# Performance work log

Measured on AMD Instinct MI355X. Metric: run time of the kernel, lower is better.

## Reference

```python
import jax, jax.numpy as jnp
import numpy as np

N = 100000; E = 200000; H = 64; P2 = 250000; P3 = 500000; G = 2048; NC = 10
NF = 18; EF = 18; Y = 0.25; EPS_BN = 1e-5


def setup_inputs() -> dict:
    key = jax.random.key(0)
    ks = jax.random.split(key, 20)
    def rn(i, shape, s=0.05):
        return jax.random.normal(ks[i], shape, jnp.float32) * s
    inp = {}
    inp["x"] = jax.random.normal(ks[0], (N, NF), jnp.float32)
    inp["edge_attr"] = jax.random.normal(ks[1], (E, EF), jnp.float32)
    inp["paths2"] = jax.random.randint(ks[2], (P2, 2), 0, N, jnp.int32)
    inp["ei2"] = jax.random.randint(ks[3], (P2, 1), 0, E, jnp.int32)
    inp["paths3"] = jax.random.randint(ks[4], (P3, 3), 0, N, jnp.int32)
    inp["ei3"] = jax.random.randint(ks[5], (P3, 2), 0, E, jnp.int32)
    inp["batch"] = jnp.sort(jax.random.randint(ks[6], (N,), 0, G, jnp.int32))
    inp["w_feat"] = rn(7, (NF, H)); inp["b_feat"] = jnp.zeros((H,), jnp.float32)
    inp["w_bond"] = rn(8, (EF, H)); inp["b_bond"] = jnp.zeros((H,), jnp.float32)
    inp["w_ih"] = rn(9, (4 * H, 2 * H)); inp["w_hh"] = rn(10, (4 * H, H))
    inp["b_ih"] = jnp.zeros((4 * H,), jnp.float32); inp["b_hh"] = jnp.zeros((4 * H,), jnp.float32)
    inp["bn_g"] = jnp.ones((2, H), jnp.float32); inp["bn_b"] = jnp.zeros((2, H), jnp.float32)
    inp["mlp_w1"] = rn(11, (2, H, H)); inp["mlp_b1"] = jnp.zeros((2, H), jnp.float32)
    inp["bn1_g"] = jnp.ones((2, H), jnp.float32); inp["bn1_b"] = jnp.zeros((2, H), jnp.float32)
    inp["mlp_w2"] = rn(12, (2, H, H)); inp["mlp_b2"] = jnp.zeros((2, H), jnp.float32)
    inp["bn2_g"] = jnp.ones((2, H), jnp.float32); inp["bn2_b"] = jnp.zeros((2, H), jnp.float32)
    inp["w_att"] = rn(13, (H,)); inp["b_att"] = jnp.zeros((1,), jnp.float32)
    inp["w_l1"] = rn(14, (H, H)); inp["b_l1"] = jnp.zeros((H,), jnp.float32)
    inp["w_l2"] = rn(15, (H, NC)); inp["b_l2"] = jnp.zeros((NC,), jnp.float32)
    return inp


def _batch_norm(x, g, b):
    # training-mode BN: biased batch statistics, eps=1e-5 (torch BatchNorm1d)
    m = x.mean(axis=0)
    v = x.var(axis=0)
    return (x - m) * jax.lax.rsqrt(v + EPS_BN) * g + b


def _lstm_final(x_seq, w_ih, w_hh, b_ih, b_hh):
    # x_seq: [P, L, 2H]; torch LSTM gate order i,f,g,o; return final hidden [P, H]
    P = x_seq.shape[0]
    Hd = w_hh.shape[1]
    def step(carry, xt):
        h, c = carry
        gates = xt @ w_ih.T + b_ih + h @ w_hh.T + b_hh
        i, f, g, o = jnp.split(gates, 4, axis=-1)
        c = jax.nn.sigmoid(f) * c + jax.nn.sigmoid(i) * jnp.tanh(g)
        h = jax.nn.sigmoid(o) * jnp.tanh(c)
        return (h, c), None
    h0 = jnp.zeros((P, Hd), x_seq.dtype)
    (h, _), _ = jax.lax.scan(step, (h0, h0), jnp.swapaxes(x_seq, 0, 1))
    return h


def _conv(i, x_in, ea_enc, paths, ei, w_ih, w_hh, b_ih, b_hh, bn_g, bn_b,
          mlp_w1, mlp_b1, bn1_g, bn1_b, mlp_w2, mlp_b2, bn2_g, bn2_b):
    P = paths.shape[0]
    ea = ea_enc[ei]                                        # [P, L-1, H]
    ea = jnp.concatenate([jnp.zeros((P, 1, H), ea.dtype), ea], axis=1)  # [P, L, H]
    x_cat = jnp.concatenate([x_in[paths], ea], axis=-1)    # [P, L, 2H]
    h = _lstm_final(x_cat, w_ih, w_hh, b_ih, b_hh)         # [P, H]
    h = jax.ops.segment_sum(h, paths[:, -1], num_segments=N)  # scatter_add to nodes
    h = _batch_norm(h, bn_g[i], bn_b[i])                   # residuals=False
    h = jax.nn.relu(_batch_norm(h @ mlp_w1[i] + mlp_b1[i], bn1_g[i], bn1_b[i]))
    h = jax.nn.relu(_batch_norm(h @ mlp_w2[i] + mlp_b2[i], bn2_g[i], bn2_b[i]))
    return h


def _attention(query, keys, w_att, b_att):
    scores = []
    for k in keys:
        s = jnp.sum(query * k, axis=0)                     # [H], sum over nodes
        s = (s - s.min()) / (s.max() - s.min() + 1e-6)
        scores.append(s @ w_att + b_att[0])                # scalar
    w = jax.nn.softmax(jnp.stack(scores))                  # [K]
    rep = sum(k * w[j] for j, k in enumerate(keys))
    return rep + query


def _forward(x, edge_attr, w_feat, b_feat, w_bond, b_bond, w_ih, w_hh, b_ih, b_hh,
             bn_g, bn_b, mlp_w1, mlp_b1, bn1_g, bn1_b, mlp_w2, mlp_b2, bn2_g, bn2_b,
             w_att, b_att, w_l1, b_l1, w_l2, b_l2, paths2, ei2, paths3, ei3, batch):
    W0 = x @ w_feat + b_feat                               # [N, H]
    ea_enc = edge_attr @ w_bond + b_bond                   # [E, H]
    common = (w_ih, w_hh, b_ih, b_hh, bn_g, bn_b, mlp_w1, mlp_b1, bn1_g, bn1_b,
              mlp_w2, mlp_b2, bn2_g, bn2_b)
    W1 = _conv(0, W0, ea_enc, paths2, ei2, *common)
    Win = (1.0 - Y) * W0 - Y * W1
    W2 = _conv(1, Win, ea_enc, paths3, ei3, *common)
    out = _attention(W0, [W1, W2], w_att, b_att)           # [N, H]
    out = jax.ops.segment_sum(out, batch, num_segments=G)  # global_add_pool -> [G, H]
    out = jax.nn.relu(out @ w_l1 + b_l1)
    return out @ w_l2 + b_l2                               # [G, NC]


def reference(x, edge_attr, paths2, ei2, paths3, ei3, batch, w_feat, b_feat,
              w_bond, b_bond, w_ih, w_hh, b_ih, b_hh, bn_g, bn_b, mlp_w1, mlp_b1,
              bn1_g, bn1_b, mlp_w2, mlp_b2, bn2_g, bn2_b, w_att, b_att,
              w_l1, b_l1, w_l2, b_l2):
    return _forward(x, edge_attr, w_feat, b_feat, w_bond, b_bond, w_ih, w_hh, b_ih, b_hh,
                    bn_g, bn_b, mlp_w1, mlp_b1, bn1_g, bn1_b, mlp_w2, mlp_b2, bn2_g, bn2_b,
                    w_att, b_att, w_l1, b_l1, w_l2, b_l2, paths2, ei2, paths3, ei3, batch)
```

## Files before the change

kernel.cpp:

```cpp
#include <hip/hip_runtime.h>
#include <math.h>

#define NNODES 100000
#define NEDGES 200000
#define HD 64
#define NP2 250000
#define NP3 500000
#define NG 2048
#define NCLS 10
#define NFEAT 18
#define EFEAT 18

typedef short short8v __attribute__((ext_vector_type(8)));
typedef float f32x4 __attribute__((ext_vector_type(4)));

__device__ __forceinline__ unsigned short bf16r(float a) {
    unsigned u = __builtin_bit_cast(unsigned, a);
    return (unsigned short)((u + 0x7FFFu + ((u >> 16) & 1u)) >> 16);
}

#define LOG2E 1.4426950408889634f

#define NB_ENC (((NNODES + NEDGES) * 64 + 255) / 256)

__global__ void prep_encode(const float* __restrict__ X, const float* __restrict__ Wf,
                            const float* __restrict__ bf,
                            const float* __restrict__ Ea, const float* __restrict__ Wb,
                            const float* __restrict__ bb,
                            float* __restrict__ W0, unsigned short* __restrict__ W0b,
                            unsigned short* __restrict__ eab,
                            const float* __restrict__ w_ih, const float* __restrict__ w_hh,
                            const float* __restrict__ b_ih, const float* __restrict__ b_hh,
                            unsigned short* __restrict__ Bp, float* __restrict__ bsum,
                            float* __restrict__ zsmall, float* __restrict__ hzero,
                            float* __restrict__ pooled) {
    int b = blockIdx.x;
    int t = threadIdx.x;
    if (b < NB_ENC) {
        long gid = (long)b * 256 + t;
        if (gid >= (long)(NNODES + NEDGES) * 64) return;
        long r = gid >> 6;
        int col = (int)(gid & 63);
        if (r < NNODES) {
            float acc = bf[col];
            const float* xr = X + r * NFEAT;
            for (int k = 0; k < NFEAT; ++k) acc += xr[k] * Wf[k * 64 + col];
            W0[gid] = acc;
            W0b[gid] = bf16r(acc);
        } else {
            long r2 = r - NNODES;
            float acc = bb[col];
            const float* xr = Ea + r2 * EFEAT;
            for (int k = 0; k < EFEAT; ++k) acc += xr[k] * Wb[k * 64 + col];
            eab[r2 * 64 + col] = bf16r(acc);
        }
    } else if (b < NB_ENC + 192) {
        int gid = (b - NB_ENC) * 256 + t;
        int kc = gid >> 13;
        int rem = gid & 8191;
        int nt = rem >> 9;
        int rem2 = rem & 511;
        int l = rem2 >> 3, j = rem2 & 7;
        int c = l & 15, q = l >> 4;
        int jh = nt >> 2, qg = nt & 3;
        int k = kc * 32 + q * 8 + j;
        int n = qg * 64 + 16 * jh + c;
        float f = (k < 128) ? w_ih[n * 128 + k] : w_hh[n * 64 + (k - 128)];
        float s = (qg == 2) ? 2.f * LOG2E : LOG2E;
        Bp[gid] = bf16r(f * s);
    } else if (b == NB_ENC + 192) {
        float s = ((t >> 6) == 2) ? 2.f * LOG2E : LOG2E;
        bsum[t] = (b_ih[t] + b_hh[t]) * s;
        for (int i = t; i < 960; i += 256) zsmall[i] = 0.f;
    } else if (b < NB_ENC + 193 + 3200) {
        long base = ((long)(b - NB_ENC - 193) * 256 + t) * 16;
        f32x4 z = {0.f, 0.f, 0.f, 0.f};
        f32x4* p = (f32x4*)(hzero + base);
        long lim = 2L * NNODES * 64;
        if (base + 16 <= lim) { p[0] = z; p[1] = z; p[2] = z; p[3] = z; }
    } else {
        pooled[(b - NB_ENC - 193 - 3200) * 256 + t] = 0.f;
    }
}

template <int L>
__global__ __launch_bounds__(256, 3)
void conv_mfma(const unsigned short* __restrict__ xb, const unsigned short* __restrict__ eab,
               const int* __restrict__ paths, const int* __restrict__ ei,
               const unsigned short* __restrict__ Bp, const float* __restrict__ bsum,
               float* __restrict__ hsum, int P) {
    __shared__ unsigned short Al[2][64 * 200];
    __shared__ int lastnode_s[64];

    const int t = threadIdx.x;
    const int w = t >> 6, lane = t & 63;
    const int c = lane & 15, q = lane >> 4;
    const int pl = t >> 2, gq = t & 3;
    const long pg = (long)blockIdx.x * 64 + pl;
    const int pc = (pg < P) ? (int)pg : P - 1;

    const short8v* __restrict__ Bv = (const short8v*)Bp;
    const int bbase = w * 256 + lane;

    float breg[4];
#pragma unroll
    for (int g2 = 0; g2 < 4; ++g2) breg[g2] = bsum[g2 * 64 + 16 * w + c];

    float creg[16];
#pragma unroll
    for (int i = 0; i < 16; ++i) creg[i] = 0.f;

    f32x4 acc[4][4];
    short8v bs0[4], bs1[4], bs2[4];
    uint4 nu0, nu1, ev0, ev1;

    {
        int node = paths[pc * L + 0];
        const uint4* s4 = (const uint4*)(xb + (size_t)node * HD);
        *(uint4*)&Al[0][pl * 200 + gq * 16] = s4[2 * gq];
        *(uint4*)&Al[0][pl * 200 + gq * 16 + 8] = s4[2 * gq + 1];
        if (gq == 0) lastnode_s[pl] = paths[pc * L + (L - 1)];
    }
    __syncthreads();

#define LOADB(BUF, KC)                                                         \
        { _Pragma("unroll")                                                    \
          for (int g2 = 0; g2 < 4; ++g2)                                       \
              BUF[g2] = Bv[(KC) * 1024 + g2 * 64 + bbase]; }

#define CHUNKS(BUF, KC)                                                        \
        { _Pragma("unroll")                                                    \
          for (int mt = 0; mt < 4; ++mt) {                                     \
              short8v af = *(const short8v*)&Ac[(mt * 16 + c) * 200 + (KC) * 32 + q * 8]; \
              _Pragma("unroll")                                                \
              for (int g2 = 0; g2 < 4; ++g2)                                   \
                  acc[mt][g2] = __builtin_amdgcn_mfma_f32_16x16x32_bf16(       \
                      af, BUF[g2], acc[mt][g2], 0, 0, 0);                      \
          } }

    int cur = 0;
    for (int step = 0; step < L; ++step) {
        const unsigned short* Ac = Al[cur];
        unsigned short* An = Al[cur ^ 1];

#pragma unroll
        for (int mt = 0; mt < 4; ++mt)
#pragma unroll
            for (int g2 = 0; g2 < 4; ++g2) {
                f32x4 v; v[0] = breg[g2]; v[1] = breg[g2]; v[2] = breg[g2]; v[3] = breg[g2];
                acc[mt][g2] = v;
            }

        if (step == 0) {
            LOADB(bs0, 0)
            LOADB(bs1, 1)
            {
                int node = paths[pc * L + 1];
                const uint4* s4 = (const uint4*)(xb + (size_t)node * HD);
                nu0 = s4[2 * gq]; nu1 = s4[2 * gq + 1];
                int e = ei[pc * (L - 1) + 0];
                const uint4* e4 = (const uint4*)(eab + (size_t)e * HD);
                ev0 = e4[2 * gq]; ev1 = e4[2 * gq + 1];
            }
            CHUNKS(bs0, 0)
            CHUNKS(bs1, 1)
        } else {
            LOADB(bs0, 0) LOADB(bs1, 1) LOADB(bs2, 2)
            CHUNKS(bs0, 0) LOADB(bs0, 3)
            CHUNKS(bs1, 1) LOADB(bs1, 4)
            CHUNKS(bs2, 2) LOADB(bs2, 5)
            if (step + 1 < L) {
                int node = paths[pc * L + step + 1];
                const uint4* s4 = (const uint4*)(xb + (size_t)node * HD);
                nu0 = s4[2 * gq]; nu1 = s4[2 * gq + 1];
                int e = ei[pc * (L - 1) + step];
                const uint4* e4 = (const uint4*)(eab + (size_t)e * HD);
                ev0 = e4[2 * gq]; ev1 = e4[2 * gq + 1];
            }
            CHUNKS(bs0, 3)
            CHUNKS(bs1, 4)
            CHUNKS(bs2, 5)
        }

#pragma unroll
        for (int mt = 0; mt < 4; ++mt) {
#pragma unroll
            for (int r = 0; r < 4; ++r) {
                float gi = acc[mt][0][r], gf = acc[mt][1][r];
                float gg = acc[mt][2][r], go = acc[mt][3][r];
                float ea = __builtin_amdgcn_exp2f(-gf);
                float eb = __builtin_amdgcn_exp2f(-gi);
                float ed = __builtin_amdgcn_exp2f(-gg);
                float eo = __builtin_amdgcn_exp2f(-go);
                float pa = 1.f + ea, pb = 1.f + eb, pd = 1.f + ed;
                float cn = (creg[mt * 4 + r] * pb * pd + (1.f - ed) * pa) *
                           __builtin_amdgcn_rcpf(pa * pb * pd);
                creg[mt * 4 + r] = cn;
                float et = __builtin_amdgcn_exp2f(-2.8853900817779268f * cn);
                float hn = (1.f - et) *
                           __builtin_amdgcn_rcpf((1.f + eo) * (1.f + et));
                if (step < L - 1) {
                    Al[cur ^ 1][(mt * 16 + q * 4 + r) * 200 + 128 + 16 * w + c] = bf16r(hn);
                } else {
                    long pr = (long)blockIdx.x * 64 + mt * 16 + q * 4 + r;
                    if (pr < P) {
                        int node = lastnode_s[mt * 16 + q * 4 + r];
                        atomicAdd(hsum + (size_t)node * HD + 16 * w + c, hn);
                    }
                }
            }
        }

        if (step + 1 < L) {
            *(uint4*)&An[pl * 200 + gq * 16] = nu0;
            *(uint4*)&An[pl * 200 + gq * 16 + 8] = nu1;
            *(uint4*)&An[pl * 200 + 64 + gq * 16] = ev0;
            *(uint4*)&An[pl * 200 + 64 + gq * 16 + 8] = ev1;
            __syncthreads();
        }
        cur ^= 1;
    }
#undef LOADB
#undef CHUNKS
}

__global__ void col_stats(const float* __restrict__ X, int nrows, float* __restrict__ out) {
    int col = threadIdx.x & 63, rg = threadIdx.x >> 6;
    float s = 0.f, q = 0.f;
    long stride = (long)gridDim.x * 4;
    for (long r = (long)blockIdx.x * 4 + rg; r < nrows; r += stride) {
        float v = X[r * 64 + col];
        s += v;
        q += v * v;
    }
    __shared__ float red[2][256];
    red[0][threadIdx.x] = s;
    red[1][threadIdx.x] = q;
    __syncthreads();
    if (threadIdx.x < 64) {
        int c = threadIdx.x;
        float ss = red[0][c] + red[0][c + 64] + red[0][c + 128] + red[0][c + 192];
        float qq = red[1][c] + red[1][c + 64] + red[1][c + 128] + red[1][c + 192];
        atomicAdd(out + c, ss);
        atomicAdd(out + 64 + c, qq);
    }
}

__device__ __forceinline__ void bn_affine(const float* stats, const float* g,
                                          const float* b, int col, int nrows,
                                          float& a, float& c) {
    float inv = 1.0f / (float)nrows;
    float mean = stats[col] * inv;
    float var = stats[64 + col] * inv - mean * mean;
    a = g[col] * rsqrtf(var + 1e-5f);
    c = b[col] - mean * a;
}

template <bool INRELU, bool STATS>
__global__ __launch_bounds__(256)
void gemm64(const float* __restrict__ X, const float* __restrict__ stats_in,
            const float* __restrict__ bn_gm, const float* __restrict__ bn_bt,
            const float* __restrict__ W, const float* __restrict__ bias,
            float* __restrict__ Y, float* stats, int nrows) {
    __shared__ float Xs[64 * 64];
    __shared__ float red[2][256];
    const int t = threadIdx.x;
    const int col = t & 63, rg = t >> 6;
    const long r0 = (long)blockIdx.x * 64;

    float a = 1.f, c = 0.f;
    if (stats_in) bn_affine(stats_in, bn_gm, bn_bt, col, nrows, a, c);

    for (int i = 0; i < 16; ++i) {
        int rl = rg * 16 + i;
        long r = r0 + rl;
        float v = (r < nrows) ? X[r * 64 + col] : 0.f;
        v = v * a + c;
        if (INRELU) v = fmaxf(v, 0.f);
        Xs[rl * 64 + col] = v;
    }
    __syncthreads();

    float wreg[64];
#pragma unroll
    for (int k = 0; k < 64; ++k) wreg[k] = W[k * 64 + col];
    float bs = bias[col];
    float ssum = 0.f, ssq = 0.f;

    for (int i = 0; i < 16; ++i) {
        int rl = rg * 16 + i;
        long r = r0 + rl;
        const float4* xs4 = (const float4*)(Xs + rl * 64);
        float acc = bs;
#pragma unroll
        for (int k4 = 0; k4 < 16; ++k4) {
            float4 xv = xs4[k4];
            acc += xv.x * wreg[4 * k4] + xv.y * wreg[4 * k4 + 1] +
                   xv.z * wreg[4 * k4 + 2] + xv.w * wreg[4 * k4 + 3];
        }
        if (r < nrows) {
            Y[r * 64 + col] = acc;
            ssum += acc;
            ssq += acc * acc;
        }
    }
    if (STATS) {
        red[0][t] = ssum;
        red[1][t] = ssq;
        __syncthreads();
        if (t < 64) {
            float s = red[0][t] + red[0][t + 64] + red[0][t + 128] + red[0][t + 192];
            float qq = red[1][t] + red[1][t + 64] + red[1][t + 128] + red[1][t + 192];
            atomicAdd(stats + t, s);
            atomicAdd(stats + 64 + t, qq);
        }
    }
}

__global__ void bn_apply1(float* __restrict__ W1, const float* __restrict__ stats,
                          const float* __restrict__ g, const float* __restrict__ b,
                          const float* __restrict__ W0, unsigned short* __restrict__ Winb,
                          long n) {
    long gid = (long)blockIdx.x * 256 + threadIdx.x;
    if (gid >= n * 64) return;
    int col = (int)(gid & 63);
    float a, c;
    bn_affine(stats, g, b, col, (int)n, a, c);
    float v = fmaxf(W1[gid] * a + c, 0.f);
    W1[gid] = v;
    Winb[gid] = bf16r(0.75f * W0[gid] - 0.25f * v);
}

__global__ void bn_apply_att(float* __restrict__ W2, const float* __restrict__ stats,
                             const float* __restrict__ g, const float* __restrict__ b,
                             const float* __restrict__ W0, const float* __restrict__ W1,
                             float* __restrict__ atts, int n) {
    int col = threadIdx.x & 63, rg = threadIdx.x >> 6;
    float a, c;
    bn_affine(stats, g, b, col, n, a, c);
    float s1 = 0.f, s2 = 0.f;
    long stride = (long)gridDim.x * 4;
    for (long r = (long)blockIdx.x * 4 + rg; r < n; r += stride) {
        long gid = r * 64 + col;
        float v = fmaxf(W2[gid] * a + c, 0.f);
        W2[gid] = v;
        float q0 = W0[gid];
        s1 += q0 * W1[gid];
        s2 += q0 * v;
    }
    __shared__ float red[2][256];
    red[0][threadIdx.x] = s1;
    red[1][threadIdx.x] = s2;
    __syncthreads();
    if (threadIdx.x < 64) {
        int cc = threadIdx.x;
        float a1 = red[0][cc] + red[0][cc + 64] + red[0][cc + 128] + red[0][cc + 192];
        float a2 = red[1][cc] + red[1][cc + 64] + red[1][cc + 128] + red[1][cc + 192];
        atomicAdd(atts + cc, a1);
        atomicAdd(atts + 64 + cc, a2);
    }
}

#define PROWS 128
__global__ void pool_rep(const float* __restrict__ W0, const float* __restrict__ W1,
                         const float* __restrict__ W2, const float* __restrict__ atts,
                         const float* __restrict__ w_att, const float* __restrict__ b_att,
                         const int* __restrict__ batch, float* __restrict__ pooled, int n) {
    __shared__ float wsh[2];
    if (threadIdx.x < 64) {
        int h = threadIdx.x;
        float z[2];
        for (int k = 0; k < 2; ++k) {
            float s = atts[64 * k + h];
            float mn = s, mx = s;
            for (int off = 32; off > 0; off >>= 1) {
                mn = fminf(mn, __shfl_down(mn, off));
                mx = fmaxf(mx, __shfl_down(mx, off));
            }
            mn = __shfl(mn, 0);
            mx = __shfl(mx, 0);
            float sn = (s - mn) / (mx - mn + 1e-6f);
            float d = sn * w_att[h];
            for (int off = 32; off > 0; off >>= 1) d += __shfl_down(d, off);
            z[k] = __shfl(d, 0) + b_att[0];
        }
        if (h == 0) {
            float m = fmaxf(z[0], z[1]);
            float e0 = expf(z[0] - m), e1 = expf(z[1] - m);
            float inv = 1.0f / (e0 + e1);
            wsh[0] = e0 * inv;
            wsh[1] = e1 * inv;
        }
    }
    __syncthreads();
    int col = threadIdx.x & 63, rg = threadIdx.x >> 6;
    long r0 = (long)blockIdx.x * PROWS;
    float w1 = wsh[0], w2 = wsh[1];
    float acc = 0.f;
    int curg = -1;
    for (int i = rg; i < PROWS; i += 4) {
        long r = r0 + i;
        if (r >= n) break;
        int g = batch[r];
        long gid = r * 64 + col;
        float rep = W0[gid] + w1 * W1[gid] + w2 * W2[gid];
        if (g != curg) {
            if (curg >= 0) atomicAdd(pooled + (size_t)curg * 64 + col, acc);
            curg = g;
            acc = 0.f;
        }
        acc += rep;
    }
    if (curg >= 0) atomicAdd(pooled + (size_t)curg * 64 + col, acc);
}

__global__ __launch_bounds__(256)
void head_kernel(const float* __restrict__ pooled, const float* __restrict__ w_l1,
                 const float* __restrict__ b_l1, const float* __restrict__ w_l2,
                 const float* __restrict__ b_l2, float* __restrict__ out) {
    __shared__ float Xs[64 * 64];
    __shared__ float Ys[64 * 65];
    const int t = threadIdx.x;
    const int col = t & 63, rg = t >> 6;
    const int r0 = blockIdx.x * 64;

    for (int i = 0; i < 16; ++i) {
        int rl = rg * 16 + i;
        Xs[rl * 64 + col] = fmaxf(pooled[(size_t)(r0 + rl) * 64 + col], 0.f);
    }
    __syncthreads();

    float wreg[64];
#pragma unroll
    for (int k = 0; k < 64; ++k) wreg[k] = w_l1[k * 64 + col];
    float bs = b_l1[col];

    for (int i = 0; i < 16; ++i) {
        int rl = rg * 16 + i;
        const float4* xs4 = (const float4*)(Xs + rl * 64);
        float acc = bs;
#pragma unroll
        for (int k4 = 0; k4 < 16; ++k4) {
            float4 xv = xs4[k4];
            acc += xv.x * wreg[4 * k4] + xv.y * wreg[4 * k4 + 1] +
                   xv.z * wreg[4 * k4 + 2] + xv.w * wreg[4 * k4 + 3];
        }
        Ys[rl * 65 + col] = fmaxf(acc, 0.f);
    }
    __syncthreads();

    for (int idx = t; idx < 64 * NCLS; idx += 256) {
        int row = idx / NCLS, j = idx - row * NCLS;
        float acc = b_l2[j];
#pragma unroll
        for (int k = 0; k < 64; ++k) acc += Ys[row * 65 + k] * w_l2[k * NCLS + j];
        out[(size_t)(r0 + row) * NCLS + j] = acc;
    }
}

extern "C" void kernel_launch(void* const* d_in, const int* in_sizes, int n_in,
                              void* d_out, int out_size, void* d_ws, size_t ws_size,
                              hipStream_t stream) {
    const float* x         = (const float*)d_in[0];
    const float* edge_attr = (const float*)d_in[1];
    const int*   paths2    = (const int*)d_in[2];
    const int*   ei2       = (const int*)d_in[3];
    const int*   paths3    = (const int*)d_in[4];
    const int*   ei3       = (const int*)d_in[5];
    const int*   batch     = (const int*)d_in[6];
    const float* w_feat    = (const float*)d_in[7];
    const float* b_feat    = (const float*)d_in[8];
    const float* w_bond    = (const float*)d_in[9];
    const float* b_bond    = (const float*)d_in[10];
    const float* w_ih      = (const float*)d_in[11];
    const float* w_hh      = (const float*)d_in[12];
    const float* b_ih      = (const float*)d_in[13];
    const float* b_hh      = (const float*)d_in[14];
    const float* bn_g      = (const float*)d_in[15];
    const float* bn_b      = (const float*)d_in[16];
    const float* mlp_w1    = (const float*)d_in[17];
    const float* mlp_b1    = (const float*)d_in[18];
    const float* bn1_g     = (const float*)d_in[19];
    const float* bn1_b     = (const float*)d_in[20];
    const float* mlp_w2    = (const float*)d_in[21];
    const float* mlp_b2    = (const float*)d_in[22];
    const float* bn2_g     = (const float*)d_in[23];
    const float* bn2_b     = (const float*)d_in[24];
    const float* w_att     = (const float*)d_in[25];
    const float* b_att     = (const float*)d_in[26];
    const float* w_l1      = (const float*)d_in[27];
    const float* b_l1      = (const float*)d_in[28];
    const float* w_l2      = (const float*)d_in[29];
    const float* b_l2      = (const float*)d_in[30];

    const size_t N64 = (size_t)NNODES * 64;
    float* ws = (float*)d_ws;
    float* W0     = ws;
    float* W1     = W0 + N64;
    float* W2     = W1 + N64;
    float* Wtmp   = W2 + N64;
    float* hsum1  = Wtmp + N64;
    float* hsum2  = hsum1 + N64;
    unsigned short* W0b  = (unsigned short*)(hsum2 + N64);
    unsigned short* Winb = W0b + N64;
    unsigned short* eab  = Winb + N64;
    unsigned short* Bp   = eab + (size_t)NEDGES * 64;
    float* bsum   = (float*)(Bp + 6 * 16 * 64 * 8);
    float* st     = bsum + 256;
    float* atts   = st + 6 * 128;
    float* watt   = atts + 128;
    float* pooled = watt + 64;
    float* outp   = (float*)d_out;

    prep_encode<<<NB_ENC + 193 + 3200 + 512, 256, 0, stream>>>(
        x, w_feat, b_feat, edge_attr, w_bond, b_bond, W0, W0b, eab,
        w_ih, w_hh, b_ih, b_hh, Bp, bsum, st, hsum1, pooled);

    conv_mfma<2><<<(NP2 + 63) / 64, 256, 0, stream>>>(W0b, eab, paths2, ei2, Bp, bsum, hsum1, NP2);

    col_stats<<<1024, 256, 0, stream>>>(hsum1, NNODES, st + 0);
    gemm64<false, true><<<(NNODES + 63) / 64, 256, 0, stream>>>(hsum1, st + 0, bn_g + 0, bn_b + 0, mlp_w1, mlp_b1, Wtmp, st + 128, NNODES);
    gemm64<true, true><<<(NNODES + 63) / 64, 256, 0, stream>>>(Wtmp, st + 128, bn1_g + 0, bn1_b + 0, mlp_w2, mlp_b2, W1, st + 256, NNODES);
    bn_apply1<<<(int)((N64 + 255) / 256), 256, 0, stream>>>(W1, st + 256, bn2_g + 0, bn2_b + 0, W0, Winb, NNODES);

    conv_mfma<3><<<(NP3 + 63) / 64, 256, 0, stream>>>(Winb, eab, paths3, ei3, Bp, bsum, hsum2, NP3);

    col_stats<<<1024, 256, 0, stream>>>(hsum2, NNODES, st + 384);
    gemm64<false, true><<<(NNODES + 63) / 64, 256, 0, stream>>>(hsum2, st + 384, bn_g + 64, bn_b + 64, mlp_w1 + 4096, mlp_b1 + 64, Wtmp, st + 512, NNODES);
    gemm64<true, true><<<(NNODES + 63) / 64, 256, 0, stream>>>(Wtmp, st + 512, bn1_g + 64, bn1_b + 64, mlp_w2 + 4096, mlp_b2 + 64, W2, st + 640, NNODES);
    bn_apply_att<<<1024, 256, 0, stream>>>(W2, st + 640, bn2_g + 64, bn2_b + 64, W0, W1, atts, NNODES);

    pool_rep<<<(NNODES + PROWS - 1) / PROWS, 256, 0, stream>>>(W0, W1, W2, atts, w_att, b_att, batch, pooled, NNODES);
    head_kernel<<<NG / 64, 256, 0, stream>>>(pooled, w_l1, b_l1, w_l2, b_l2, outp);
}
```

Measured before the change: 712.3 us.

## Precompute first LSTM step per node instead of per path

The first LSTM step depends only on the starting node's features (zero initial state), so a new init_state kernel computes h and c for every node once. The path conv kernels then gather the precomputed h (bf16) and c (fp32) for each path's first node and start the recurrence at step 1. This replaces per-path first-step MFMA work (250k and 500k paths) with work over 100k nodes, at the cost of an extra launch and extra gather traffic for h0 and c0. c0 reuses the W2 buffer as scratch.

```diff
diff --git a/kernel.cpp b/kernel.cpp
--- a/kernel.cpp
+++ b/kernel.cpp
@@ -83,14 +83,93 @@
     }
 }
 
+__global__ __launch_bounds__(256)
+void init_state(const unsigned short* __restrict__ xb,
+                const unsigned short* __restrict__ Bp, const float* __restrict__ bsum,
+                unsigned short* __restrict__ h0b, float* __restrict__ c0) {
+    __shared__ unsigned short Al[64 * 200];
+    const int t = threadIdx.x;
+    const int w = t >> 6, lane = t & 63;
+    const int c = lane & 15, q = lane >> 4;
+    const int pl = t >> 2, gq = t & 3;
+    const int r0 = blockIdx.x * 64;
+    const short8v* __restrict__ Bv = (const short8v*)Bp;
+    const int bbase = w * 256 + lane;
+
+    {
+        int row = r0 + pl;
+        if (row >= NNODES) row = NNODES - 1;
+        const uint4* s4 = (const uint4*)(xb + (size_t)row * HD);
+        *(uint4*)&Al[pl * 200 + gq * 16] = s4[2 * gq];
+        *(uint4*)&Al[pl * 200 + gq * 16 + 8] = s4[2 * gq + 1];
+    }
+    float breg[4];
+#pragma unroll
+    for (int g2 = 0; g2 < 4; ++g2) breg[g2] = bsum[g2 * 64 + 16 * w + c];
+    __syncthreads();
+
+    short8v b0[4], b1[4];
+#pragma unroll
+    for (int g2 = 0; g2 < 4; ++g2) {
+        b0[g2] = Bv[g2 * 64 + bbase];
+        b1[g2] = Bv[1024 + g2 * 64 + bbase];
+    }
+    f32x4 acc[4][4];
+#pragma unroll
+    for (int mt = 0; mt < 4; ++mt)
+#pragma unroll
+        for (int g2 = 0; g2 < 4; ++g2) {
+            f32x4 v; v[0] = breg[g2]; v[1] = breg[g2]; v[2] = breg[g2]; v[3] = breg[g2];
+            acc[mt][g2] = v;
+        }
+#pragma unroll
+    for (int mt = 0; mt < 4; ++mt) {
+        short8v af = *(const short8v*)&Al[(mt * 16 + c) * 200 + q * 8];
+#pragma unroll
+        for (int g2 = 0; g2 < 4; ++g2)
+            acc[mt][g2] = __builtin_amdgcn_mfma_f32_16x16x32_bf16(af, b0[g2], acc[mt][g2], 0, 0, 0);
+    }
+#pragma unroll
+    for (int mt = 0; mt < 4; ++mt) {
+        short8v af = *(const short8v*)&Al[(mt * 16 + c) * 200 + 32 + q * 8];
+#pragma unroll
+        for (int g2 = 0; g2 < 4; ++g2)
+            acc[mt][g2] = __builtin_amdgcn_mfma_f32_16x16x32_bf16(af, b1[g2], acc[mt][g2], 0, 0, 0);
+    }
+
+#pragma unroll
+    for (int mt = 0; mt < 4; ++mt) {
+#pragma unroll
+        for (int r = 0; r < 4; ++r) {
+            float gi = acc[mt][0][r], gf = acc[mt][1][r];
+            float gg = acc[mt][2][r], go = acc[mt][3][r];
+            float ea = __builtin_amdgcn_exp2f(-gf);
+            float eb = __builtin_amdgcn_exp2f(-gi);
+            float ed = __builtin_amdgcn_exp2f(-gg);
+            float eo = __builtin_amdgcn_exp2f(-go);
+            float pa = 1.f + ea, pb = 1.f + eb, pd = 1.f + ed;
+            float cn = ((1.f - ed) * pa) * __builtin_amdgcn_rcpf(pa * pb * pd);
+            float et = __builtin_amdgcn_exp2f(-2.8853900817779268f * cn);
+            float hn = (1.f - et) * __builtin_amdgcn_rcpf((1.f + eo) * (1.f + et));
+            int node = r0 + mt * 16 + q * 4 + r;
+            if (node < NNODES) {
+                h0b[(size_t)node * HD + 16 * w + c] = bf16r(hn);
+                c0[(size_t)node * HD + 16 * w + c] = cn;
+            }
+        }
+    }
+}
+
 template <int L>
 __global__ __launch_bounds__(256, 3)
 void conv_mfma(const unsigned short* __restrict__ xb, const unsigned short* __restrict__ eab,
+               const unsigned short* __restrict__ h0b, const float* __restrict__ c0,
                const int* __restrict__ paths, const int* __restrict__ ei,
                const unsigned short* __restrict__ Bp, const float* __restrict__ bsum,
                float* __restrict__ hsum, int P) {
     __shared__ unsigned short Al[2][64 * 200];
     __shared__ int lastnode_s[64];
+    __shared__ int firstnode_s[64];
 
     const int t = threadIdx.x;
     const int w = t >> 6, lane = t & 63;
@@ -107,21 +186,34 @@
     for (int g2 = 0; g2 < 4; ++g2) breg[g2] = bsum[g2 * 64 + 16 * w + c];
 
     float creg[16];
-#pragma unroll
-    for (int i = 0; i < 16; ++i) creg[i] = 0.f;
-
     f32x4 acc[4][4];
     short8v bs0[4], bs1[4], bs2[4];
     uint4 nu0, nu1, ev0, ev1;
 
     {
-        int node = paths[pc * L + 0];
-        const uint4* s4 = (const uint4*)(xb + (size_t)node * HD);
+        int n0 = paths[pc * L + 0];
+        int n1 = paths[pc * L + 1];
+        int e0 = ei[pc * (L - 1) + 0];
+        const uint4* s4 = (const uint4*)(xb + (size_t)n1 * HD);
         *(uint4*)&Al[0][pl * 200 + gq * 16] = s4[2 * gq];
         *(uint4*)&Al[0][pl * 200 + gq * 16 + 8] = s4[2 * gq + 1];
+        const uint4* e4 = (const uint4*)(eab + (size_t)e0 * HD);
+        *(uint4*)&Al[0][pl * 200 + 64 + gq * 16] = e4[2 * gq];
+        *(uint4*)&Al[0][pl * 200 + 64 + gq * 16 + 8] = e4[2 * gq + 1];
+        const uint4* h4 = (const uint4*)(h0b + (size_t)n0 * HD);
+        *(uint4*)&Al[0][pl * 200 + 128 + gq * 16] = h4[2 * gq];
+        *(uint4*)&Al[0][pl * 200 + 128 + gq * 16 + 8] = h4[2 * gq + 1];
         if (gq == 0) lastnode_s[pl] = paths[pc * L + (L - 1)];
-    }
-    __syncthreads();
+        if (gq == 1) firstnode_s[pl] = n0;
+    }
+    __syncthreads();
+
+#pragma unroll
+    for (int mt = 0; mt < 4; ++mt)
+#pragma unroll
+        for (int r = 0; r < 4; ++r)
+            creg[mt * 4 + r] =
+                c0[(size_t)firstnode_s[mt * 16 + q * 4 + r] * HD + 16 * w + c];
 
 #define LOADB(BUF, KC)                                                         \
         { _Pragma("unroll")                                                    \
@@ -139,7 +231,7 @@
           } }
 
     int cur = 0;
-    for (int step = 0; step < L; ++step) {
+    for (int step = 1; step < L; ++step) {
         const unsigned short* Ac = Al[cur];
         unsigned short* An = Al[cur ^ 1];
 
@@ -151,36 +243,21 @@
                 acc[mt][g2] = v;
             }
 
-        if (step == 0) {
-            LOADB(bs0, 0)
-            LOADB(bs1, 1)
-            {
-                int node = paths[pc * L + 1];
-                const uint4* s4 = (const uint4*)(xb + (size_t)node * HD);
-                nu0 = s4[2 * gq]; nu1 = s4[2 * gq + 1];
-                int e = ei[pc * (L - 1) + 0];
-                const uint4* e4 = (const uint4*)(eab + (size_t)e * HD);
-                ev0 = e4[2 * gq]; ev1 = e4[2 * gq + 1];
-            }
-            CHUNKS(bs0, 0)
-            CHUNKS(bs1, 1)
-        } else {
-            LOADB(bs0, 0) LOADB(bs1, 1) LOADB(bs2, 2)
-            CHUNKS(bs0, 0) LOADB(bs0, 3)
-            CHUNKS(bs1, 1) LOADB(bs1, 4)
-            CHUNKS(bs2, 2) LOADB(bs2, 5)
-            if (step + 1 < L) {
-                int node = paths[pc * L + step + 1];
-                const uint4* s4 = (const uint4*)(xb + (size_t)node * HD);
-                nu0 = s4[2 * gq]; nu1 = s4[2 * gq + 1];
-                int e = ei[pc * (L - 1) + step];
-                const uint4* e4 = (const uint4*)(eab + (size_t)e * HD);
-                ev0 = e4[2 * gq]; ev1 = e4[2 * gq + 1];
-            }
-            CHUNKS(bs0, 3)
-            CHUNKS(bs1, 4)
-            CHUNKS(bs2, 5)
-        }
+        LOADB(bs0, 0) LOADB(bs1, 1) LOADB(bs2, 2)
+        CHUNKS(bs0, 0) LOADB(bs0, 3)
+        CHUNKS(bs1, 1) LOADB(bs1, 4)
+        CHUNKS(bs2, 2) LOADB(bs2, 5)
+        if (step + 1 < L) {
+            int node = paths[pc * L + step + 1];
+            const uint4* s4 = (const uint4*)(xb + (size_t)node * HD);
+            nu0 = s4[2 * gq]; nu1 = s4[2 * gq + 1];
+            int e = ei[pc * (L - 1) + step];
+            const uint4* e4 = (const uint4*)(eab + (size_t)e * HD);
+            ev0 = e4[2 * gq]; ev1 = e4[2 * gq + 1];
+        }
+        CHUNKS(bs0, 3)
+        CHUNKS(bs1, 4)
+        CHUNKS(bs2, 5)
 
 #pragma unroll
         for (int mt = 0; mt < 4; ++mt) {
@@ -200,7 +277,7 @@
                 float hn = (1.f - et) *
                            __builtin_amdgcn_rcpf((1.f + eo) * (1.f + et));
                 if (step < L - 1) {
-                    Al[cur ^ 1][(mt * 16 + q * 4 + r) * 200 + 128 + 16 * w + c] = bf16r(hn);
+                    An[(mt * 16 + q * 4 + r) * 200 + 128 + 16 * w + c] = bf16r(hn);
                 } else {
                     long pr = (long)blockIdx.x * 64 + mt * 16 + q * 4 + r;
                     if (pr < P) {
@@ -510,20 +587,24 @@
     float* atts   = st + 6 * 128;
     float* watt   = atts + 128;
     float* pooled = watt + 64;
+    unsigned short* h0b = (unsigned short*)(pooled + (size_t)NG * 64);
+    float* c0 = W2;
     float* outp   = (float*)d_out;
 
     prep_encode<<<NB_ENC + 193 + 3200 + 512, 256, 0, stream>>>(
         x, w_feat, b_feat, edge_attr, w_bond, b_bond, W0, W0b, eab,
         w_ih, w_hh, b_ih, b_hh, Bp, bsum, st, hsum1, pooled);
 
-    conv_mfma<2><<<(NP2 + 63) / 64, 256, 0, stream>>>(W0b, eab, paths2, ei2, Bp, bsum, hsum1, NP2);
+    init_state<<<(NNODES + 63) / 64, 256, 0, stream>>>(W0b, Bp, bsum, h0b, c0);
+    conv_mfma<2><<<(NP2 + 63) / 64, 256, 0, stream>>>(W0b, eab, h0b, c0, paths2, ei2, Bp, bsum, hsum1, NP2);
 
     col_stats<<<1024, 256, 0, stream>>>(hsum1, NNODES, st + 0);
     gemm64<false, true><<<(NNODES + 63) / 64, 256, 0, stream>>>(hsum1, st + 0, bn_g + 0, bn_b + 0, mlp_w1, mlp_b1, Wtmp, st + 128, NNODES);
     gemm64<true, true><<<(NNODES + 63) / 64, 256, 0, stream>>>(Wtmp, st + 128, bn1_g + 0, bn1_b + 0, mlp_w2, mlp_b2, W1, st + 256, NNODES);
     bn_apply1<<<(int)((N64 + 255) / 256), 256, 0, stream>>>(W1, st + 256, bn2_g + 0, bn2_b + 0, W0, Winb, NNODES);
 
-    conv_mfma<3><<<(NP3 + 63) / 64, 256, 0, stream>>>(Winb, eab, paths3, ei3, Bp, bsum, hsum2, NP3);
+    init_state<<<(NNODES + 63) / 64, 256, 0, stream>>>(Winb, Bp, bsum, h0b, c0);
+    conv_mfma<3><<<(NP3 + 63) / 64, 256, 0, stream>>>(Winb, eab, h0b, c0, paths3, ei3, Bp, bsum, hsum2, NP3);
 
     col_stats<<<1024, 256, 0, stream>>>(hsum2, NNODES, st + 384);
     gemm64<false, true><<<(NNODES + 63) / 64, 256, 0, stream>>>(hsum2, st + 384, bn_g + 64, bn_b + 64, mlp_w1 + 4096, mlp_b1 + 64, Wtmp, st + 512, NNODES);
```

New measurement: 801.5 us. 1.13x slower.
